# Performance work log

Measured on AMD Instinct MI355X. Metric: run time of the kernel, lower is better.

## Reference

```python
import jax, jax.numpy as jnp
import numpy as np

N, E, M = 8192, 32768, 2048
D, H1, C = 768, 8, 768
NEG_SLOPE = 0.2


def gat_conv(x, src, dst, W, att_src, att_dst, bias, heads, out_ch):
    # PyG GATConv (eval mode, concat=True, add_self_loops already applied to src/dst)
    n = x.shape[0]
    h = (x @ W).reshape(n, heads, out_ch)                      # [N,H,C]
    a_src = jnp.einsum('nhc,hc->nh', h, att_src)               # [N,H]
    a_dst = jnp.einsum('nhc,hc->nh', h, att_dst)
    e = jax.nn.leaky_relu(a_src[src] + a_dst[dst], NEG_SLOPE)  # [E',H]
    # softmax over incoming edges of each dst node
    m = jax.ops.segment_max(e, dst, num_segments=n)
    e = jnp.exp(e - m[dst])
    denom = jax.ops.segment_sum(e, dst, num_segments=n)
    alpha = e / (denom[dst] + 1e-16)                           # [E',H]
    msg = h[src] * alpha[:, :, None]                           # [E',H,C]
    out = jax.ops.segment_sum(msg, dst, num_segments=n)        # [N,H,C]
    return out.reshape(n, heads * out_ch) + bias


def setup_inputs() -> dict:
    key = jax.random.key(0)
    ks = jax.random.split(key, 16)
    s = 0.02
    inp = {
        'x': jax.random.normal(ks[0], (N, D), jnp.float32),
        'edge_index': jax.random.randint(ks[1], (2, E), 0, N, jnp.int64),
        'mask_idx': jax.random.randint(ks[2], (M,), 0, N, jnp.int64),
        'W1': jax.random.normal(ks[3], (D, H1 * C), jnp.float32) * s,
        'att_src1': jax.random.normal(ks[4], (H1, C), jnp.float32) * s,
        'att_dst1': jax.random.normal(ks[5], (H1, C), jnp.float32) * s,
        'b1': jnp.zeros((H1 * C,), jnp.float32),
        'W2': jax.random.normal(ks[6], (H1 * C, C), jnp.float32) * s,
        'att_src2': jax.random.normal(ks[7], (1, C), jnp.float32) * s,
        'att_dst2': jax.random.normal(ks[8], (1, C), jnp.float32) * s,
        'b2': jnp.zeros((C,), jnp.float32),
        # fc: 1536 -> 768, classifier: 768 -> 2
        'fc_w': jax.random.normal(ks[9], (2 * C, C), jnp.float32) * s,
        'fc_b': jnp.zeros((C,), jnp.float32),
        'cls_w': jax.random.normal(ks[10], (C, 2), jnp.float32) * s,
        'cls_b': jnp.zeros((2,), jnp.float32),
    }
    return inp


def reference(x, edge_index, mask_idx, W1, att_src1, att_dst1, b1,
              W2, att_src2, att_dst2, b2, fc_w, fc_b, cls_w, cls_b):
    n = x.shape[0]
    loops = jnp.arange(n, dtype=edge_index.dtype)
    src = jnp.concatenate([edge_index[0], loops])   # PyG default add_self_loops
    dst = jnp.concatenate([edge_index[1], loops])
    h = gat_conv(x, src, dst, W1, att_src1, att_dst1, b1, H1, C)   # [N, 6144]
    h = jax.nn.elu(h)
    h = gat_conv(h, src, dst, W2, att_src2, att_dst2, b2, 1, C)    # [N, 768]
    x_gemb = h[mask_idx]                                           # [M, 768]
    x_emb = x[mask_idx]                                            # [M, 768]
    out = jnp.concatenate([x_gemb, x_emb], axis=1) @ fc_w + fc_b   # [M, 768]
    out = out @ cls_w + cls_b                                      # [M, 2]
    return out
```

## Files before the change

kernel.cpp:

```cpp
#include <hip/hip_runtime.h>

typedef unsigned short ushort_t;
typedef __attribute__((ext_vector_type(8))) __bf16 bf16x8;
typedef __attribute__((ext_vector_type(8))) unsigned short ushort8;
typedef __attribute__((ext_vector_type(4))) unsigned short ushort4v;
typedef __attribute__((ext_vector_type(4))) float f32x4;

#define N_NODES 8192
#define NODE_MASK 8191
#define E_EDGES 32768
#define E_TOT   40960
#define M_MASK  2048
#define D_IN    768
#define C_CH    768
#define F1      6144

typedef __attribute__((address_space(1))) const void* gas_ptr;
typedef __attribute__((address_space(3))) void* las_ptr;

__device__ __forceinline__ float bf2f(ushort_t u) {
    union { unsigned int i; float f; } v; v.i = ((unsigned int)u) << 16; return v.f;
}
__device__ __forceinline__ ushort_t f2bf(float f) {
    union { float f; unsigned int i; } v; v.f = f;
    unsigned int r = v.i + 0x7fffu + ((v.i >> 16) & 1u);
    return (ushort_t)(r >> 16);
}

__global__ void init_kernel(int* deg, int* fill, int* flags) {
    int i = blockIdx.x * 256 + threadIdx.x;
    if (i < N_NODES) { deg[i] = 0; fill[i] = 0; }
    if (i < 2) flags[i] = 0;
}
__global__ void detect_kernel(const int* __restrict__ raw, int nhalf, int* __restrict__ flag) {
    int i = blockIdx.x * 256 + threadIdx.x;
    if (i < nhalf && raw[2 * i + 1] != 0) atomicOr(flag, 1);
}
__global__ void convert_idx_kernel(const void* __restrict__ raw, int n,
                                   const int* __restrict__ flag, int* __restrict__ out) {
    int i = blockIdx.x * 256 + threadIdx.x;
    if (i >= n) return;
    int v = (*flag) ? ((const int*)raw)[i] : (int)((const long long*)raw)[i];
    out[i] = v & NODE_MASK;
}

__global__ void cvt_bf16_kernel(const float* __restrict__ in, ushort_t* __restrict__ out, int n4) {
    int i = blockIdx.x * 256 + threadIdx.x;
    if (i >= n4) return;
    f32x4 v = *(const f32x4*)(in + i * 4);
    ushort_t o0 = f2bf(v[0]), o1 = f2bf(v[1]), o2 = f2bf(v[2]), o3 = f2bf(v[3]);
    unsigned long long pk = (unsigned long long)o0 | ((unsigned long long)o1 << 16)
                          | ((unsigned long long)o2 << 32) | ((unsigned long long)o3 << 48);
    *(unsigned long long*)(out + i * 4) = pk;
}

__global__ __launch_bounds__(256) void transpose_cvt_kernel(
    const float* __restrict__ in, ushort_t* __restrict__ out, int R, int Ccols)
{
    __shared__ ushort_t tile[32][33];
    int tx = threadIdx.x & 31, ty = threadIdx.x >> 5;
    int x  = blockIdx.x * 32 + tx;
    int y0 = blockIdx.y * 32;
#pragma unroll
    for (int i = 0; i < 4; ++i)
        tile[ty + i * 8][tx] = f2bf(in[(size_t)(y0 + ty + i * 8) * Ccols + x]);
    __syncthreads();
#pragma unroll
    for (int i = 0; i < 4; ++i)
        out[(size_t)(blockIdx.x * 32 + ty + i * 8) * R + y0 + tx] = tile[tx][ty + i * 8];
}

__global__ __launch_bounds__(256) void gemm_bt_kernel(
    const ushort_t* __restrict__ A, const ushort_t* __restrict__ Bt,
    ushort_t* __restrict__ C, const float* __restrict__ bias,
    int M, int N, int K)
{
    __shared__ ushort_t lsA[128 * 64];
    __shared__ ushort_t lsB[128 * 64];

    const int tid  = threadIdx.x;
    const int lane = tid & 63;
    const int wave = tid >> 6;
    const int wm = wave >> 1, wn = wave & 1;
    const int bx = blockIdx.x, by = blockIdx.y;

    const f32x4 zero = {0.f, 0.f, 0.f, 0.f};
    f32x4 acc[4][4];
#pragma unroll
    for (int i = 0; i < 4; ++i)
#pragma unroll
        for (int j = 0; j < 4; ++j) acc[i][j] = zero;

    const int l8 = lane >> 3;
    const int c8 = lane & 7;
    const int q  = lane >> 4;
    const int rl = lane & 15;

    for (int kt = 0; kt < K; kt += 64) {
        __syncthreads();
#pragma unroll
        for (int i = 0; i < 4; ++i) {
            int rbase = wave * 32 + i * 8;
            int row   = rbase + l8;
            int gch   = c8 ^ (row & 7);
            const ushort_t* gA = A  + (size_t)(by * 128 + row) * K + kt + gch * 8;
            const ushort_t* gB = Bt + (size_t)(bx * 128 + row) * K + kt + gch * 8;
            __builtin_amdgcn_global_load_lds((gas_ptr)gA, (las_ptr)(lsA + rbase * 64), 16, 0, 0);
            __builtin_amdgcn_global_load_lds((gas_ptr)gB, (las_ptr)(lsB + rbase * 64), 16, 0, 0);
        }
        __syncthreads();
#pragma unroll
        for (int s = 0; s < 2; ++s) {
            bf16x8 af[4], bfv[4];
#pragma unroll
            for (int i = 0; i < 4; ++i) {
                int Ra = wm * 64 + i * 16 + rl;
                af[i]  = *(const bf16x8*)(lsA + Ra * 64 + (((s * 4 + q) ^ (Ra & 7)) * 8));
                int Rb = wn * 64 + i * 16 + rl;
                bfv[i] = *(const bf16x8*)(lsB + Rb * 64 + (((s * 4 + q) ^ (Rb & 7)) * 8));
            }
#pragma unroll
            for (int i = 0; i < 4; ++i)
#pragma unroll
                for (int j = 0; j < 4; ++j)
                    acc[i][j] = __builtin_amdgcn_mfma_f32_16x16x32_bf16(af[i], bfv[j], acc[i][j], 0, 0, 0);
        }
    }
#pragma unroll
    for (int j = 0; j < 4; ++j) {
        int col = bx * 128 + wn * 64 + j * 16 + rl;
        float bv = bias ? bias[col] : 0.0f;
#pragma unroll
        for (int i = 0; i < 4; ++i) {
#pragma unroll
            for (int t = 0; t < 4; ++t) {
                int row = by * 128 + wm * 64 + i * 16 + q * 4 + t;
                C[(size_t)row * N + col] = f2bf(acc[i][j][t] + bv);
            }
        }
    }
}

#define NBX2 6
#define NBY2 64
#define NSPLIT 2

__global__ __launch_bounds__(256) void gemm_bt_splitk_kernel(
    const ushort_t* __restrict__ A, const ushort_t* __restrict__ Bt,
    float* __restrict__ Cpart, int M, int N, int K)
{
    __shared__ ushort_t lsA[128 * 64];
    __shared__ ushort_t lsB[128 * 64];

    const int tid  = threadIdx.x;
    const int lane = tid & 63;
    const int wave = tid >> 6;
    const int wm = wave >> 1, wn = wave & 1;

    const int d    = blockIdx.x;
    const int xcd  = d & 7;
    const int slot = d >> 3;
    const int bx   = slot % NBX2;
    const int grp  = xcd * 16 + slot / NBX2;
    const int by   = grp & (NBY2 - 1);
    const int bz   = grp >> 6;

    const int kh  = K >> 1;
    const int kt0 = bz * kh;
    float* __restrict__ Cp = Cpart + (size_t)bz * M * N;

    const f32x4 zero = {0.f, 0.f, 0.f, 0.f};
    f32x4 acc[4][4];
#pragma unroll
    for (int i = 0; i < 4; ++i)
#pragma unroll
        for (int j = 0; j < 4; ++j) acc[i][j] = zero;

    const int l8 = lane >> 3;
    const int c8 = lane & 7;
    const int q  = lane >> 4;
    const int rl = lane & 15;

    for (int kt = kt0; kt < kt0 + kh; kt += 64) {
        __syncthreads();
#pragma unroll
        for (int i = 0; i < 4; ++i) {
            int rbase = wave * 32 + i * 8;
            int row   = rbase + l8;
            int gch   = c8 ^ (row & 7);
            const ushort_t* gA = A  + (size_t)(by * 128 + row) * K + kt + gch * 8;
            const ushort_t* gB = Bt + (size_t)(bx * 128 + row) * K + kt + gch * 8;
            __builtin_amdgcn_global_load_lds((gas_ptr)gA, (las_ptr)(lsA + rbase * 64), 16, 0, 0);
            __builtin_amdgcn_global_load_lds((gas_ptr)gB, (las_ptr)(lsB + rbase * 64), 16, 0, 0);
        }
        __syncthreads();
#pragma unroll
        for (int s = 0; s < 2; ++s) {
            bf16x8 af[4], bfv[4];
#pragma unroll
            for (int i = 0; i < 4; ++i) {
                int Ra = wm * 64 + i * 16 + rl;
                af[i]  = *(const bf16x8*)(lsA + Ra * 64 + (((s * 4 + q) ^ (Ra & 7)) * 8));
                int Rb = wn * 64 + i * 16 + rl;
                bfv[i] = *(const bf16x8*)(lsB + Rb * 64 + (((s * 4 + q) ^ (Rb & 7)) * 8));
            }
#pragma unroll
            for (int i = 0; i < 4; ++i)
#pragma unroll
                for (int j = 0; j < 4; ++j)
                    acc[i][j] = __builtin_amdgcn_mfma_f32_16x16x32_bf16(af[i], bfv[j], acc[i][j], 0, 0, 0);
        }
    }
#pragma unroll
    for (int j = 0; j < 4; ++j) {
        int col = bx * 128 + wn * 64 + j * 16 + rl;
#pragma unroll
        for (int i = 0; i < 4; ++i) {
#pragma unroll
            for (int t = 0; t < 4; ++t) {
                int row = by * 128 + wm * 64 + i * 16 + q * 4 + t;
                Cp[(size_t)row * N + col] = acc[i][j][t];
            }
        }
    }
}

__global__ __launch_bounds__(192) void splitk_reduce_att_kernel(
    const float* __restrict__ P0, const float* __restrict__ P1,
    ushort_t* __restrict__ out, const float* __restrict__ as2,
    const float* __restrict__ ad2, float* __restrict__ a_s, float* __restrict__ a_d)
{
    const int n = blockIdx.x, tid = threadIdx.x;
    const int c0 = tid * 4;
    f32x4 a = *(const f32x4*)(P0 + (size_t)n * C_CH + c0);
    f32x4 b = *(const f32x4*)(P1 + (size_t)n * C_CH + c0);
    f32x4 ws = *(const f32x4*)(as2 + c0);
    f32x4 wd = *(const f32x4*)(ad2 + c0);
    float s1 = 0.f, s2 = 0.f;
    ushort_t o[4];
#pragma unroll
    for (int k = 0; k < 4; ++k) {
        float v = a[k] + b[k];
        o[k] = f2bf(v);
        s1 += v * ws[k];
        s2 += v * wd[k];
    }
    unsigned long long pk = (unsigned long long)o[0] | ((unsigned long long)o[1] << 16)
                          | ((unsigned long long)o[2] << 32) | ((unsigned long long)o[3] << 48);
    *(unsigned long long*)(out + (size_t)n * C_CH + c0) = pk;

    __shared__ float red[2][3];
#pragma unroll
    for (int off = 32; off > 0; off >>= 1) {
        s1 += __shfl_down(s1, off);
        s2 += __shfl_down(s2, off);
    }
    const int lane = tid & 63, wv = tid >> 6;
    if (lane == 0) { red[0][wv] = s1; red[1][wv] = s2; }
    __syncthreads();
    if (tid == 0) {
        a_s[n] = red[0][0] + red[0][1] + red[0][2];
        a_d[n] = red[1][0] + red[1][1] + red[1][2];
    }
}

__global__ void indeg_kernel(const int* __restrict__ eic, int* __restrict__ deg) {
    int e = blockIdx.x * 256 + threadIdx.x;
    if (e >= E_TOT) return;
    int dst = (e < E_EDGES) ? eic[E_EDGES + e] : (e - E_EDGES);
    atomicAdd(&deg[dst], 1);
}
__global__ __launch_bounds__(256) void scan_kernel(const int* __restrict__ deg, int* __restrict__ rowptr) {
    __shared__ int part[256];
    int t = threadIdx.x;
    int local[32];
    int s = 0;
#pragma unroll
    for (int i = 0; i < 32; ++i) { local[i] = deg[t * 32 + i]; s += local[i]; }
    part[t] = s;
    __syncthreads();
    for (int off = 1; off < 256; off <<= 1) {
        int v = (t >= off) ? part[t - off] : 0;
        __syncthreads();
        part[t] += v;
        __syncthreads();
    }
    int run = (t == 0) ? 0 : part[t - 1];
#pragma unroll
    for (int i = 0; i < 32; ++i) { rowptr[t * 32 + i] = run; run += local[i]; }
    if (t == 255) rowptr[N_NODES] = run;
}
__global__ void scatter_kernel(const int* __restrict__ eic, const int* __restrict__ rowptr,
                               int* __restrict__ fill, int* __restrict__ csr_src) {
    int e = blockIdx.x * 256 + threadIdx.x;
    if (e >= E_TOT) return;
    int src, dst;
    if (e < E_EDGES) { src = eic[e]; dst = eic[E_EDGES + e]; }
    else             { src = e - E_EDGES; dst = src; }
    int pos = rowptr[dst] + atomicAdd(&fill[dst], 1);
    csr_src[pos] = src;
}

__global__ __launch_bounds__(256) void att1_wprep_kernel(
    const float* __restrict__ W1, const float* __restrict__ att_s,
    const float* __restrict__ att_d, float* __restrict__ ws, float* __restrict__ wd)
{
    int gid  = blockIdx.x * 4 + (threadIdx.x >> 6);
    int lane = threadIdx.x & 63;
    int d = gid >> 3, h = gid & 7;
    const float* wp = W1 + (size_t)d * F1 + h * C_CH;
    const float* sp = att_s + h * C_CH;
    const float* dp = att_d + h * C_CH;
    float s1 = 0.f, s2 = 0.f;
#pragma unroll
    for (int j = 0; j < 3; ++j) {
        int o = j * 256 + lane * 4;
        f32x4 w  = *(const f32x4*)(wp + o);
        f32x4 sv = *(const f32x4*)(sp + o);
        f32x4 dv = *(const f32x4*)(dp + o);
#pragma unroll
        for (int k = 0; k < 4; ++k) { s1 += w[k] * sv[k]; s2 += w[k] * dv[k]; }
    }
#pragma unroll
    for (int off = 32; off > 0; off >>= 1) {
        s1 += __shfl_down(s1, off);
        s2 += __shfl_down(s2, off);
    }
    if (lane == 0) { ws[h * D_IN + d] = s1; wd[h * D_IN + d] = s2; }
}

__global__ __launch_bounds__(256) void att1_gemv_kernel(
    const ushort_t* __restrict__ xb, const float* __restrict__ ws,
    const float* __restrict__ wd, float* __restrict__ a_s, float* __restrict__ a_d)
{
    int n    = blockIdx.x * 4 + (threadIdx.x >> 6);
    int lane = threadIdx.x & 63;
    const ushort_t* xp = xb + (size_t)n * D_IN;
    float s[8], d[8];
#pragma unroll
    for (int h = 0; h < 8; ++h) { s[h] = 0.f; d[h] = 0.f; }
#pragma unroll
    for (int j = 0; j < 3; ++j) {
        int d0 = j * 256 + lane * 4;
        ushort4v xv = *(const ushort4v*)(xp + d0);
        float xf0 = bf2f(xv[0]), xf1 = bf2f(xv[1]), xf2 = bf2f(xv[2]), xf3 = bf2f(xv[3]);
#pragma unroll
        for (int h = 0; h < 8; ++h) {
            f32x4 wv = *(const f32x4*)(ws + (size_t)h * D_IN + d0);
            f32x4 dv = *(const f32x4*)(wd + (size_t)h * D_IN + d0);
            s[h] += xf0 * wv[0] + xf1 * wv[1] + xf2 * wv[2] + xf3 * wv[3];
            d[h] += xf0 * dv[0] + xf1 * dv[1] + xf2 * dv[2] + xf3 * dv[3];
        }
    }
#pragma unroll
    for (int h = 0; h < 8; ++h) {
#pragma unroll
        for (int off = 32; off > 0; off >>= 1) {
            s[h] += __shfl_down(s[h], off);
            d[h] += __shfl_down(d[h], off);
        }
    }
    if (lane == 0) {
#pragma unroll
        for (int h = 0; h < 8; ++h) { a_s[n * 8 + h] = s[h]; a_d[n * 8 + h] = d[h]; }
    }
}

__global__ __launch_bounds__(192) void agg8_kernel(
    const ushort_t* __restrict__ h, const float* __restrict__ a_s, const float* __restrict__ a_d,
    const int* __restrict__ rowptr, const int* __restrict__ csr_src,
    const float* __restrict__ bias, ushort_t* __restrict__ out)
{
    const int n = blockIdx.x;
    const int half = blockIdx.y;
    const int tid = threadIdx.x;
    const int base = rowptr[n];
    const int deg  = rowptr[n + 1] - base;

    __shared__ float s_m[8], s_rd[8], s_adst[8];
    __shared__ int   s_src[64];
    __shared__ float s_w[64][8];

    if (tid < 8) {
        float adst = a_d[n * 8 + tid];
        float m = -1e30f;
        for (int e = 0; e < deg; ++e) {
            float scv = a_s[csr_src[base + e] * 8 + tid] + adst;
            scv = scv > 0.f ? scv : 0.2f * scv;
            m = fmaxf(m, scv);
        }
        float den = 0.f;
        for (int e = 0; e < deg; ++e) {
            float scv = a_s[csr_src[base + e] * 8 + tid] + adst;
            scv = scv > 0.f ? scv : 0.2f * scv;
            den += __expf(scv - m);
        }
        s_m[tid] = m; s_rd[tid] = 1.0f / (den + 1e-16f); s_adst[tid] = adst;
    }
    __syncthreads();

    float acc[16];
#pragma unroll
    for (int i = 0; i < 16; ++i) acc[i] = 0.f;
    const int c0   = half * 3072 + tid * 16;
    const int myhd = (half << 2) + tid / 48;

    for (int cs = 0; cs < deg; cs += 64) {
        int cnt = min(64, deg - cs);
        __syncthreads();
        for (int idx = tid; idx < cnt; idx += 192) s_src[idx] = csr_src[base + cs + idx];
        __syncthreads();
        for (int idx = tid; idx < cnt * 8; idx += 192) {
            int e = idx >> 3, hd = idx & 7;
            float scv = a_s[s_src[e] * 8 + hd] + s_adst[hd];
            scv = scv > 0.f ? scv : 0.2f * scv;
            s_w[e][hd] = __expf(scv - s_m[hd]) * s_rd[hd];
        }
        __syncthreads();
        int e = 0;
        for (; e + 1 < cnt; e += 2) {
            const ushort_t* hp0 = h + (size_t)s_src[e] * F1 + c0;
            const ushort_t* hp1 = h + (size_t)s_src[e + 1] * F1 + c0;
            ushort8 a0 = *(const ushort8*)(hp0);
            ushort8 a1 = *(const ushort8*)(hp0 + 8);
            ushort8 b0 = *(const ushort8*)(hp1);
            ushort8 b1 = *(const ushort8*)(hp1 + 8);
            float w0 = s_w[e][myhd], w1 = s_w[e + 1][myhd];
#pragma unroll
            for (int i = 0; i < 8; ++i) {
                acc[i]     += w0 * bf2f(a0[i]) + w1 * bf2f(b0[i]);
                acc[8 + i] += w0 * bf2f(a1[i]) + w1 * bf2f(b1[i]);
            }
        }
        if (e < cnt) {
            const ushort_t* hp0 = h + (size_t)s_src[e] * F1 + c0;
            ushort8 a0 = *(const ushort8*)(hp0);
            ushort8 a1 = *(const ushort8*)(hp0 + 8);
            float w0 = s_w[e][myhd];
#pragma unroll
            for (int i = 0; i < 8; ++i) {
                acc[i]     += w0 * bf2f(a0[i]);
                acc[8 + i] += w0 * bf2f(a1[i]);
            }
        }
    }
#pragma unroll
    for (int i = 0; i < 16; ++i) {
        float v = acc[i] + bias[c0 + i];
        v = v > 0.f ? v : (__expf(v) - 1.0f);
        out[(size_t)n * F1 + c0 + i] = f2bf(v);
    }
}

__global__ __launch_bounds__(256) void agg1_kernel(
    const ushort_t* __restrict__ h, const float* __restrict__ a_s, const float* __restrict__ a_d,
    const int* __restrict__ rowptr, const int* __restrict__ csr_src,
    const float* __restrict__ bias, ushort_t* __restrict__ out)
{
    const int n    = blockIdx.x * 4 + (threadIdx.x >> 6);
    const int lane = threadIdx.x & 63;
    const int base = rowptr[n];
    const int deg  = rowptr[n + 1] - base;
    const float adst = a_d[n];

    float m = -1e30f;
    for (int cs = 0; cs < deg; cs += 64) {
        int e = cs + lane;
        if (e < deg) {
            float scv = a_s[csr_src[base + e]] + adst;
            scv = scv > 0.f ? scv : 0.2f * scv;
            m = fmaxf(m, scv);
        }
    }
#pragma unroll
    for (int off = 32; off > 0; off >>= 1) m = fmaxf(m, __shfl_xor(m, off));
    float den = 0.f;
    for (int cs = 0; cs < deg; cs += 64) {
        int e = cs + lane;
        if (e < deg) {
            float scv = a_s[csr_src[base + e]] + adst;
            scv = scv > 0.f ? scv : 0.2f * scv;
            den += __expf(scv - m);
        }
    }
#pragma unroll
    for (int off = 32; off > 0; off >>= 1) den += __shfl_xor(den, off);
    const float rd = 1.0f / (den + 1e-16f);

    const int c0 = lane * 12;
    float acc[12];
#pragma unroll
    for (int i = 0; i < 12; ++i) acc[i] = 0.f;

    for (int cs = 0; cs < deg; cs += 64) {
        int cnt = min(64, deg - cs);
        int e = cs + lane;
        int srcl = (e < deg) ? csr_src[base + e] : 0;
        float wv = 0.f;
        if (e < deg) {
            float scv = a_s[srcl] + adst;
            scv = scv > 0.f ? scv : 0.2f * scv;
            wv = __expf(scv - m) * rd;
        }
        for (int k = 0; k < cnt; ++k) {
            int src = __shfl(srcl, k);
            float w = __shfl(wv, k);
            const ushort_t* hp = h + (size_t)src * C_CH + c0;
            ushort4v v0 = *(const ushort4v*)(hp);
            ushort4v v1 = *(const ushort4v*)(hp + 4);
            ushort4v v2 = *(const ushort4v*)(hp + 8);
#pragma unroll
            for (int i = 0; i < 4; ++i) {
                acc[i]     += w * bf2f(v0[i]);
                acc[4 + i] += w * bf2f(v1[i]);
                acc[8 + i] += w * bf2f(v2[i]);
            }
        }
    }
#pragma unroll
    for (int p = 0; p < 3; ++p) {
        ushort_t o0 = f2bf(acc[p * 4 + 0] + bias[c0 + p * 4 + 0]);
        ushort_t o1 = f2bf(acc[p * 4 + 1] + bias[c0 + p * 4 + 1]);
        ushort_t o2 = f2bf(acc[p * 4 + 2] + bias[c0 + p * 4 + 2]);
        ushort_t o3 = f2bf(acc[p * 4 + 3] + bias[c0 + p * 4 + 3]);
        unsigned long long pk = (unsigned long long)o0 | ((unsigned long long)o1 << 16)
                              | ((unsigned long long)o2 << 32) | ((unsigned long long)o3 << 48);
        *(unsigned long long*)(out + (size_t)n * C_CH + c0 + p * 4) = pk;
    }
}

__global__ void gatherfc_kernel(const ushort_t* __restrict__ out2, const ushort_t* __restrict__ xb,
                                const int* __restrict__ maskc, ushort_t* __restrict__ Afc)
{
    int m = blockIdx.x, t = threadIdx.x;
    int mi = maskc[m];
    const ushort_t* p1 = out2 + (size_t)mi * 768;
    const ushort_t* p2 = xb   + (size_t)mi * 768;
    for (int c = t; c < 768; c += 256) {
        Afc[(size_t)m * 1536 + c]       = p1[c];
        Afc[(size_t)m * 1536 + 768 + c] = p2[c];
    }
}

__global__ __launch_bounds__(256) void cls_kernel(
    const ushort_t* __restrict__ fc_out, const float* __restrict__ cls_w,
    const float* __restrict__ cls_b, float* __restrict__ out)
{
    int m = blockIdx.x * 4 + (threadIdx.x >> 6);
    int lane = threadIdx.x & 63;
    float a0 = 0.f, a1 = 0.f;
    const ushort_t* row = fc_out + (size_t)m * 768;
    for (int i = lane; i < 768; i += 64) {
        float v = bf2f(row[i]);
        a0 += v * cls_w[i * 2 + 0];
        a1 += v * cls_w[i * 2 + 1];
    }
#pragma unroll
    for (int off = 32; off > 0; off >>= 1) {
        a0 += __shfl_down(a0, off);
        a1 += __shfl_down(a1, off);
    }
    if (lane == 0) {
        out[m * 2 + 0] = a0 + cls_b[0];
        out[m * 2 + 1] = a1 + cls_b[1];
    }
}

extern "C" void kernel_launch(void* const* d_in, const int* in_sizes, int n_in,
                              void* d_out, int out_size, void* d_ws, size_t ws_size,
                              hipStream_t stream)
{
    const float* x        = (const float*)d_in[0];
    const void*  ei_raw   = d_in[1];
    const void*  mask_raw = d_in[2];
    const float* W1       = (const float*)d_in[3];
    const float* att_src1 = (const float*)d_in[4];
    const float* att_dst1 = (const float*)d_in[5];
    const float* b1       = (const float*)d_in[6];
    const float* W2       = (const float*)d_in[7];
    const float* att_src2 = (const float*)d_in[8];
    const float* att_dst2 = (const float*)d_in[9];
    const float* b2       = (const float*)d_in[10];
    const float* fc_w     = (const float*)d_in[11];
    const float* fc_b     = (const float*)d_in[12];
    const float* cls_w    = (const float*)d_in[13];
    const float* cls_b    = (const float*)d_in[14];
    float* out = (float*)d_out;

    char* ws = (char*)d_ws;
    size_t off = 0;
    auto alloc = [&](size_t bytes) { char* p = ws + off; off = (off + bytes + 255) & ~(size_t)255; return p; };
    int*   flags  = (int*)alloc(2 * 4);
    int*   eic    = (int*)alloc((size_t)2 * E_EDGES * 4);
    int*   maskc  = (int*)alloc((size_t)M_MASK * 4);
    int*   deg    = (int*)alloc(N_NODES * 4);
    int*   fill   = (int*)alloc(N_NODES * 4);
    int*   rowptr = (int*)alloc((N_NODES + 1) * 4);
    int*   csr    = (int*)alloc(E_TOT * 4);
    float* a_s1   = (float*)alloc((size_t)N_NODES * 8 * 4);
    float* a_d1   = (float*)alloc((size_t)N_NODES * 8 * 4);
    float* a_s2   = (float*)alloc((size_t)N_NODES * 4);
    float* a_d2   = (float*)alloc((size_t)N_NODES * 4);
    float* ws1    = (float*)alloc((size_t)D_IN * 8 * 4);
    float* wd1    = (float*)alloc((size_t)D_IN * 8 * 4);
    ushort_t* W1t  = (ushort_t*)alloc((size_t)D_IN * F1 * 2);
    ushort_t* W2t  = (ushort_t*)alloc((size_t)F1 * C_CH * 2);
    ushort_t* fcwt = (ushort_t*)alloc((size_t)1536 * 768 * 2);
    ushort_t* xb   = (ushort_t*)alloc((size_t)N_NODES * D_IN * 2);
    char* region1 = alloc((size_t)N_NODES * F1 * 2);
    char* region2 = alloc((size_t)N_NODES * F1 * 2);
    ushort_t* h1    = (ushort_t*)region1;
    ushort_t* h2    = (ushort_t*)region1;
    ushort_t* Afc   = (ushort_t*)(region1 + (16u << 20));
    ushort_t* fcout = (ushort_t*)(region1 + (32u << 20));
    float*    part  = (float*)(region1 + (48u << 20));
    ushort_t* out1  = (ushort_t*)region2;
    ushort_t* out2  = (ushort_t*)region2;

    init_kernel<<<N_NODES / 256, 256, 0, stream>>>(deg, fill, flags);
    detect_kernel<<<(E_EDGES + 255) / 256, 256, 0, stream>>>((const int*)ei_raw, E_EDGES, &flags[0]);
    detect_kernel<<<(M_MASK / 2 + 255) / 256, 256, 0, stream>>>((const int*)mask_raw, M_MASK / 2, &flags[1]);
    convert_idx_kernel<<<(2 * E_EDGES + 255) / 256, 256, 0, stream>>>(ei_raw, 2 * E_EDGES, &flags[0], eic);
    convert_idx_kernel<<<(M_MASK + 255) / 256, 256, 0, stream>>>(mask_raw, M_MASK, &flags[1], maskc);
    indeg_kernel<<<E_TOT / 256, 256, 0, stream>>>(eic, deg);
    scan_kernel<<<1, 256, 0, stream>>>(deg, rowptr);
    scatter_kernel<<<E_TOT / 256, 256, 0, stream>>>(eic, rowptr, fill, csr);

    cvt_bf16_kernel<<<(N_NODES * D_IN / 4 + 255) / 256, 256, 0, stream>>>(x, xb, N_NODES * D_IN / 4);
    att1_wprep_kernel<<<(D_IN * 8) / 4, 256, 0, stream>>>(W1, att_src1, att_dst1, ws1, wd1);
    att1_gemv_kernel<<<N_NODES / 4, 256, 0, stream>>>(xb, ws1, wd1, a_s1, a_d1);
    transpose_cvt_kernel<<<dim3(F1 / 32, D_IN / 32), 256, 0, stream>>>(W1, W1t, D_IN, F1);
    transpose_cvt_kernel<<<dim3(C_CH / 32, F1 / 32), 256, 0, stream>>>(W2, W2t, F1, C_CH);
    transpose_cvt_kernel<<<dim3(768 / 32, 1536 / 32), 256, 0, stream>>>(fc_w, fcwt, 1536, 768);

    gemm_bt_kernel<<<dim3(F1 / 128, N_NODES / 128), 256, 0, stream>>>(xb, W1t, h1, nullptr, N_NODES, F1, D_IN);
    agg8_kernel<<<dim3(N_NODES, 2), 192, 0, stream>>>(h1, a_s1, a_d1, rowptr, csr, b1, out1);

    gemm_bt_splitk_kernel<<<NBX2 * NBY2 * NSPLIT, 256, 0, stream>>>(out1, W2t, part, N_NODES, C_CH, F1);
    splitk_reduce_att_kernel<<<N_NODES, 192, 0, stream>>>(
        part, part + (size_t)N_NODES * C_CH, h2, att_src2, att_dst2, a_s2, a_d2);
    agg1_kernel<<<N_NODES / 4, 256, 0, stream>>>(h2, a_s2, a_d2, rowptr, csr, b2, out2);

    gatherfc_kernel<<<M_MASK, 256, 0, stream>>>(out2, xb, maskc, Afc);
    gemm_bt_kernel<<<dim3(768 / 128, M_MASK / 128), 256, 0, stream>>>(Afc, fcwt, fcout, fc_b, M_MASK, 768, 1536);
    cls_kernel<<<M_MASK / 4, 256, 0, stream>>>(fcout, cls_w, cls_b, out);
}
```

Measured before the change: 511.8 us.

## Aggregate raw features per head before projecting with W1 in layer one

Layer one now runs aggregation first: for each node and each of the 8 heads it sums the attention-weighted 768-wide bf16 input features into an [8,N,768] buffer. A batched per-head GEMM against the matching W1 slice then produces the output, with bias and ELU fused into its epilogue. The aim is to stop gathering 6144-wide rows of h1 per edge and to drop the h1 write-then-read round trip. GEMM FLOPs stay about the same. The cost is an extra bf16 rounding of the aggregated features, and the aggregation step does 8x more FMAs per feature element loaded.

```diff
diff --git a/kernel.cpp b/kernel.cpp
--- a/kernel.cpp
+++ b/kernel.cpp
@@ -136,6 +136,82 @@
             for (int t = 0; t < 4; ++t) {
                 int row = by * 128 + wm * 64 + i * 16 + q * 4 + t;
                 C[(size_t)row * N + col] = f2bf(acc[i][j][t] + bv);
+            }
+        }
+    }
+}
+
+__global__ __launch_bounds__(256) void gemm_bd_kernel(
+    const ushort_t* __restrict__ A0, const ushort_t* __restrict__ Bt0,
+    ushort_t* __restrict__ C, const float* __restrict__ bias,
+    int M, int K)
+{
+    __shared__ ushort_t lsA[128 * 64];
+    __shared__ ushort_t lsB[128 * 64];
+
+    const int tid  = threadIdx.x;
+    const int lane = tid & 63;
+    const int wave = tid >> 6;
+    const int wm = wave >> 1, wn = wave & 1;
+    const int bx = blockIdx.x, by = blockIdx.y, head = blockIdx.z;
+
+    const ushort_t* A  = A0  + (size_t)head * M * K;
+    const ushort_t* Bt = Bt0 + (size_t)head * C_CH * K;
+
+    const f32x4 zero = {0.f, 0.f, 0.f, 0.f};
+    f32x4 acc[4][4];
+#pragma unroll
+    for (int i = 0; i < 4; ++i)
+#pragma unroll
+        for (int j = 0; j < 4; ++j) acc[i][j] = zero;
+
+    const int l8 = lane >> 3;
+    const int c8 = lane & 7;
+    const int q  = lane >> 4;
+    const int rl = lane & 15;
+
+    for (int kt = 0; kt < K; kt += 64) {
+        __syncthreads();
+#pragma unroll
+        for (int i = 0; i < 4; ++i) {
+            int rbase = wave * 32 + i * 8;
+            int row   = rbase + l8;
+            int gch   = c8 ^ (row & 7);
+            const ushort_t* gA = A  + (size_t)(by * 128 + row) * K + kt + gch * 8;
+            const ushort_t* gB = Bt + (size_t)(bx * 128 + row) * K + kt + gch * 8;
+            __builtin_amdgcn_global_load_lds((gas_ptr)gA, (las_ptr)(lsA + rbase * 64), 16, 0, 0);
+            __builtin_amdgcn_global_load_lds((gas_ptr)gB, (las_ptr)(lsB + rbase * 64), 16, 0, 0);
+        }
+        __syncthreads();
+#pragma unroll
+        for (int s = 0; s < 2; ++s) {
+            bf16x8 af[4], bfv[4];
+#pragma unroll
+            for (int i = 0; i < 4; ++i) {
+                int Ra = wm * 64 + i * 16 + rl;
+                af[i]  = *(const bf16x8*)(lsA + Ra * 64 + (((s * 4 + q) ^ (Ra & 7)) * 8));
+                int Rb = wn * 64 + i * 16 + rl;
+                bfv[i] = *(const bf16x8*)(lsB + Rb * 64 + (((s * 4 + q) ^ (Rb & 7)) * 8));
+            }
+#pragma unroll
+            for (int i = 0; i < 4; ++i)
+#pragma unroll
+                for (int j = 0; j < 4; ++j)
+                    acc[i][j] = __builtin_amdgcn_mfma_f32_16x16x32_bf16(af[i], bfv[j], acc[i][j], 0, 0, 0);
+        }
+    }
+#pragma unroll
+    for (int j = 0; j < 4; ++j) {
+        int colf = head * C_CH + bx * 128 + wn * 64 + j * 16 + rl;
+        float bv = bias[colf];
+#pragma unroll
+        for (int i = 0; i < 4; ++i) {
+#pragma unroll
+            for (int t = 0; t < 4; ++t) {
+                int row = by * 128 + wm * 64 + i * 16 + q * 4 + t;
+                float v = acc[i][j][t] + bv;
+                v = v > 0.f ? v : (__expf(v) - 1.0f);
+                C[(size_t)row * F1 + colf] = f2bf(v);
             }
         }
     }
@@ -366,13 +442,12 @@
     }
 }
 
-__global__ __launch_bounds__(192) void agg8_kernel(
-    const ushort_t* __restrict__ h, const float* __restrict__ a_s, const float* __restrict__ a_d,
+__global__ __launch_bounds__(192) void agg8x_kernel(
+    const ushort_t* __restrict__ xb, const float* __restrict__ a_s, const float* __restrict__ a_d,
     const int* __restrict__ rowptr, const int* __restrict__ csr_src,
-    const float* __restrict__ bias, ushort_t* __restrict__ out)
+    ushort_t* __restrict__ xagg)
 {
     const int n = blockIdx.x;
-    const int half = blockIdx.y;
     const int tid = threadIdx.x;
     const int base = rowptr[n];
     const int deg  = rowptr[n + 1] - base;
@@ -399,11 +474,12 @@
     }
     __syncthreads();
 
-    float acc[16];
-#pragma unroll
-    for (int i = 0; i < 16; ++i) acc[i] = 0.f;
-    const int c0   = half * 3072 + tid * 16;
-    const int myhd = (half << 2) + tid / 48;
+    float acc[8][4];
+#pragma unroll
+    for (int h = 0; h < 8; ++h)
+#pragma unroll
+        for (int i = 0; i < 4; ++i) acc[h][i] = 0.f;
+    const int c0 = tid * 4;
 
     for (int cs = 0; cs < deg; cs += 64) {
         int cnt = min(64, deg - cs);
@@ -417,38 +493,27 @@
             s_w[e][hd] = __expf(scv - s_m[hd]) * s_rd[hd];
         }
         __syncthreads();
-        int e = 0;
-        for (; e + 1 < cnt; e += 2) {
-            const ushort_t* hp0 = h + (size_t)s_src[e] * F1 + c0;
-            const ushort_t* hp1 = h + (size_t)s_src[e + 1] * F1 + c0;
-            ushort8 a0 = *(const ushort8*)(hp0);
-            ushort8 a1 = *(const ushort8*)(hp0 + 8);
-            ushort8 b0 = *(const ushort8*)(hp1);
-            ushort8 b1 = *(const ushort8*)(hp1 + 8);
-            float w0 = s_w[e][myhd], w1 = s_w[e + 1][myhd];
-#pragma unroll
-            for (int i = 0; i < 8; ++i) {
-                acc[i]     += w0 * bf2f(a0[i]) + w1 * bf2f(b0[i]);
-                acc[8 + i] += w0 * bf2f(a1[i]) + w1 * bf2f(b1[i]);
+        for (int e = 0; e < cnt; ++e) {
+            const ushort_t* xp = xb + (size_t)s_src[e] * D_IN + c0;
+            ushort4v xv = *(const ushort4v*)(xp);
+            float xf0 = bf2f(xv[0]), xf1 = bf2f(xv[1]), xf2 = bf2f(xv[2]), xf3 = bf2f(xv[3]);
+#pragma unroll
+            for (int h = 0; h < 8; ++h) {
+                float w = s_w[e][h];
+                acc[h][0] += w * xf0;
+                acc[h][1] += w * xf1;
+                acc[h][2] += w * xf2;
+                acc[h][3] += w * xf3;
             }
         }
-        if (e < cnt) {
-            const ushort_t* hp0 = h + (size_t)s_src[e] * F1 + c0;
-            ushort8 a0 = *(const ushort8*)(hp0);
-            ushort8 a1 = *(const ushort8*)(hp0 + 8);
-            float w0 = s_w[e][myhd];
-#pragma unroll
-            for (int i = 0; i < 8; ++i) {
-                acc[i]     += w0 * bf2f(a0[i]);
-                acc[8 + i] += w0 * bf2f(a1[i]);
-            }
-        }
-    }
-#pragma unroll
-    for (int i = 0; i < 16; ++i) {
-        float v = acc[i] + bias[c0 + i];
-        v = v > 0.f ? v : (__expf(v) - 1.0f);
-        out[(size_t)n * F1 + c0 + i] = f2bf(v);
+    }
+#pragma unroll
+    for (int h = 0; h < 8; ++h) {
+        ushort_t o0 = f2bf(acc[h][0]), o1 = f2bf(acc[h][1]);
+        ushort_t o2 = f2bf(acc[h][2]), o3 = f2bf(acc[h][3]);
+        unsigned long long pk = (unsigned long long)o0 | ((unsigned long long)o1 << 16)
+                              | ((unsigned long long)o2 << 32) | ((unsigned long long)o3 << 48);
+        *(unsigned long long*)(xagg + ((size_t)h * N_NODES + n) * D_IN + c0) = pk;
     }
 }
 
@@ -609,7 +674,7 @@
     ushort_t* xb   = (ushort_t*)alloc((size_t)N_NODES * D_IN * 2);
     char* region1 = alloc((size_t)N_NODES * F1 * 2);
     char* region2 = alloc((size_t)N_NODES * F1 * 2);
-    ushort_t* h1    = (ushort_t*)region1;
+    ushort_t* xagg  = (ushort_t*)region1;
     ushort_t* h2    = (ushort_t*)region1;
     ushort_t* Afc   = (ushort_t*)(region1 + (16u << 20));
     ushort_t* fcout = (ushort_t*)(region1 + (32u << 20));
@@ -633,8 +698,9 @@
     transpose_cvt_kernel<<<dim3(C_CH / 32, F1 / 32), 256, 0, stream>>>(W2, W2t, F1, C_CH);
     transpose_cvt_kernel<<<dim3(768 / 32, 1536 / 32), 256, 0, stream>>>(fc_w, fcwt, 1536, 768);
 
-    gemm_bt_kernel<<<dim3(F1 / 128, N_NODES / 128), 256, 0, stream>>>(xb, W1t, h1, nullptr, N_NODES, F1, D_IN);
-    agg8_kernel<<<dim3(N_NODES, 2), 192, 0, stream>>>(h1, a_s1, a_d1, rowptr, csr, b1, out1);
+    agg8x_kernel<<<N_NODES, 192, 0, stream>>>(xb, a_s1, a_d1, rowptr, csr, xagg);
+    gemm_bd_kernel<<<dim3(C_CH / 128, N_NODES / 128, 8), 256, 0, stream>>>(
+        xagg, W1t, out1, b1, N_NODES, D_IN);
 
     gemm_bt_splitk_kernel<<<NBX2 * NBY2 * NSPLIT, 256, 0, stream>>>(out1, W2t, part, N_NODES, C_CH, F1);
     splitk_reduce_att_kernel<<<N_NODES, 192, 0, stream>>>(
```

Result: faster. 494.6 us (-3.4%).
